# Kernel optimization log

Hardware: AMD Instinct MI355X
Metric: run time of the kernel (lower is better)

The kernel has to match this reference:

```python
import jax, jax.numpy as jnp
import numpy as np
import math

D_MODEL = 1024
N_HEADS = 16
D_HEAD = D_MODEL // N_HEADS
WINDOW = 256
SCALE = 1.0 / math.sqrt(D_HEAD)


def setup_inputs() -> dict:
    key = jax.random.key(0)
    kx, kqkv, kout = jax.random.split(key, 3)
    x = jax.random.normal(kx, (2, 2048, D_MODEL), dtype=jnp.float32)
    # xavier_uniform for nn.Linear weights (shape [out, in] in torch; store as [in, out] for x @ W)
    lim_qkv = math.sqrt(6.0 / (D_MODEL + 3 * D_MODEL))
    W_qkv = jax.random.uniform(kqkv, (D_MODEL, 3 * D_MODEL), dtype=jnp.float32, minval=-lim_qkv, maxval=lim_qkv)
    lim_out = math.sqrt(6.0 / (D_MODEL + D_MODEL))
    W_out = jax.random.uniform(kout, (D_MODEL, D_MODEL), dtype=jnp.float32, minval=-lim_out, maxval=lim_out)
    return {"x": x, "W_qkv": W_qkv, "W_out": W_out}


def _window_mask(seq_len: int) -> jnp.ndarray:
    # causal + sliding window: position i attends to j with i-WINDOW < j <= i
    i = jnp.arange(seq_len)[:, None]
    j = jnp.arange(seq_len)[None, :]
    allowed = (j <= i) & (j > i - WINDOW)
    return jnp.where(allowed, 0.0, -jnp.inf).astype(jnp.float32)


def reference(x, W_qkv, W_out):
    B, S, _ = x.shape
    qkv = x @ W_qkv                                   # [B, S, 3*D]
    qkv = qkv.reshape(B, S, 3, N_HEADS, D_HEAD)
    qkv = jnp.transpose(qkv, (2, 0, 3, 1, 4))         # [3, B, H, S, Dh]
    q, k, v = qkv[0], qkv[1], qkv[2]
    scores = jnp.einsum('bhsd,bhtd->bhst', q, k) * SCALE
    scores = scores + _window_mask(S)[None, None]
    weights = jax.nn.softmax(scores, axis=-1)
    out = jnp.einsum('bhst,bhtd->bhsd', weights, v)   # [B, H, S, Dh]
    out = jnp.transpose(out, (0, 2, 1, 3)).reshape(B, S, D_MODEL)
    return out @ W_out
```

## Files before the change

### kernel.cpp

```cpp
#include <hip/hip_runtime.h>

typedef unsigned short u16;
typedef unsigned int u32;

#define D_MODEL 1024
#define N_HEADS 16
#define D_HEAD 64
#define WIN 256
#define SEQ 2048
#define BATCH 2
#define NROWS (BATCH*SEQ)

typedef short frag_ab __attribute__((ext_vector_type(8)));
typedef float frag_cd __attribute__((ext_vector_type(4)));
typedef float f32x16 __attribute__((ext_vector_type(16)));
typedef u16 u16x8 __attribute__((ext_vector_type(8)));

__device__ __forceinline__ u16 f2bf(float f) {
    union { float f; u32 u; } x; x.f = f;
    u32 r = x.u + 0x7fffu + ((x.u >> 16) & 1u);
    return (u16)(r >> 16);
}

__device__ __forceinline__ void load_lds16(const void* g, void* l) {
    __builtin_amdgcn_global_load_lds(
        (const __attribute__((address_space(1))) void*)g,
        (__attribute__((address_space(3))) void*)l, 16, 0, 0);
}

__device__ __forceinline__ void transpose_tile(const float* __restrict__ W, u16* __restrict__ WT,
                                               int K, int N, int n0, int k0,
                                               int scale_rows, float scale, float (*tile)[33]) {
    int x = threadIdx.x & 31, y = threadIdx.x >> 5;
#pragma unroll
    for (int r = 0; r < 4; r++)
        tile[y + 8 * r][x] = W[(size_t)(k0 + y + 8 * r) * N + n0 + x];
    __syncthreads();
#pragma unroll
    for (int r = 0; r < 4; r++) {
        int nrow = n0 + y + 8 * r;
        float v = tile[x][y + 8 * r];
        if (nrow < scale_rows) v *= scale;
        WT[(size_t)nrow * K + k0 + x] = f2bf(v);
    }
}

__global__ __launch_bounds__(256) void prep_kernel(const float* __restrict__ x,
                                                   const float* __restrict__ W_qkv,
                                                   u16* __restrict__ xb,
                                                   u16* __restrict__ wqkvT,
                                                   float qscale) {
    __shared__ float tile[32][33];
    const int bid = blockIdx.x;
    if (bid < 4096) {
        int idx = bid * 256 + threadIdx.x;
        float4 v = ((const float4*)x)[idx];
        ushort4 o;
        o.x = f2bf(v.x); o.y = f2bf(v.y); o.z = f2bf(v.z); o.w = f2bf(v.w);
        ((ushort4*)xb)[idx] = o;
    } else {
        int t = bid - 4096;
        transpose_tile(W_qkv, wqkvT, D_MODEL, 3 * D_MODEL, (t % 96) * 32, (t / 96) * 32,
                       D_MODEL, qscale, tile);
    }
}

__global__ __launch_bounds__(512, 2) void gemm1_qkv(const u16* __restrict__ A,
                                                    const u16* __restrict__ BT,
                                                    u16* __restrict__ C) {
    constexpr int K = 1024, NLD = 3072, NT = K >> 6;
    __shared__ union SM {
        struct { u16 As[2][256 * 64]; u16 Bs[2][192 * 64]; } s;
        u16 cs[256 * 200];
    } sm;
    const int tid = threadIdx.x;
    const int xcd = blockIdx.x & 7, sblk = blockIdx.x >> 3;
    const int m0 = (sblk & 15) * 256;
    const int n0 = (xcd * 2 + (sblk >> 4)) * 192;
    const int wave = tid >> 6, lane = tid & 63;
    const int wm = (wave >> 1) * 64, wn = (wave & 1) * 96;
    const int l32 = lane & 31, kh = lane >> 5;

    const int r0 = tid >> 3;
    const int w  = (tid & 7) ^ (r0 & 7);
    const u16* aP = A  + (size_t)(m0 + r0) * K + w * 8;
    const u16* bP = BT + (size_t)(n0 + r0) * K + w * 8;

    f32x16 acc[2][3] = {};

#define STAGE(tile_, buf_) do {                                                   \
        const int k0_ = (tile_) * 64;                                             \
        _Pragma("unroll")                                                         \
        for (int u = 0; u < 4; ++u)                                               \
            load_lds16(aP + (size_t)(64 * u) * K + k0_,                           \
                       &sm.s.As[buf_][(tid + 512 * u) * 8]);                      \
        _Pragma("unroll")                                                         \
        for (int u = 0; u < 3; ++u)                                               \
            load_lds16(bP + (size_t)(64 * u) * K + k0_,                           \
                       &sm.s.Bs[buf_][(tid + 512 * u) * 8]);                      \
    } while (0)

    STAGE(0, 0);
    STAGE(1, 1);

    int cur = 0;
    for (int t = 0; t < NT; ++t) {
        if (t + 1 < NT) asm volatile("s_waitcnt vmcnt(7)" ::: "memory");
        else            asm volatile("s_waitcnt vmcnt(0)" ::: "memory");
        asm volatile("s_barrier" ::: "memory");

        const u16* As = sm.s.As[cur];
        const u16* Bs = sm.s.Bs[cur];
#pragma unroll
        for (int kk = 0; kk < 4; ++kk) {
            const int csel = ((kk * 2 + kh) ^ (l32 & 7)) * 8;
            frag_ab af[2], bf[3];
#pragma unroll
            for (int mt = 0; mt < 2; ++mt)
                af[mt] = *(const frag_ab*)&As[(wm + mt * 32 + l32) * 64 + csel];
#pragma unroll
            for (int nt = 0; nt < 3; ++nt)
                bf[nt] = *(const frag_ab*)&Bs[(wn + nt * 32 + l32) * 64 + csel];
            asm volatile("s_barrier" ::: "memory");
            __builtin_amdgcn_s_setprio(1);
#pragma unroll
            for (int mt = 0; mt < 2; ++mt)
#pragma unroll
                for (int nt = 0; nt < 3; ++nt)
                    acc[mt][nt] = __builtin_amdgcn_mfma_f32_32x32x16_bf16(
                        af[mt], bf[nt], acc[mt][nt], 0, 0, 0);
            __builtin_amdgcn_s_setprio(0);
            asm volatile("s_barrier" ::: "memory");
        }
        if (t + 2 < NT) STAGE(t + 2, cur);
        cur ^= 1;
    }
#undef STAGE

#pragma unroll
    for (int mt = 0; mt < 2; ++mt)
#pragma unroll
        for (int nt = 0; nt < 3; ++nt) {
            const int col = wn + nt * 32 + l32;
#pragma unroll
            for (int reg = 0; reg < 16; ++reg) {
                const int row = wm + mt * 32 + (reg & 3) + 8 * (reg >> 2) + 4 * kh;
                sm.cs[row * 200 + col] = f2bf(acc[mt][nt][reg]);
            }
        }
    asm volatile("s_barrier" ::: "memory");
#pragma unroll
    for (int i = 0; i < 12; ++i) {
        const int idx = tid + 512 * i;
        const int row = idx / 24, c8 = idx % 24;
        u16x8 vv = *(const u16x8*)&sm.cs[row * 200 + c8 * 8];
        *(u16x8*)(C + (size_t)(m0 + row) * NLD + n0 + c8 * 8) = vv;
    }
}

__global__ __launch_bounds__(256) void gemm2_out(const u16* __restrict__ A,
                                                 const u16* __restrict__ BT,
                                                 float* __restrict__ C) {
    constexpr int K = 1024, N = 1024, NT = K >> 6;
    __shared__ struct { u16 As[2][128 * 64]; u16 Bs[2][128 * 64]; } sm;
    const int tid = threadIdx.x;
    const int xcd = blockIdx.x & 7, sblk = blockIdx.x >> 3;
    const int m0 = sblk * 128;
    const int n0 = xcd * 128;
    const int wave = tid >> 6, lane = tid & 63;
    const int wm = (wave >> 1) * 64, wn = (wave & 1) * 64;
    const int l32 = lane & 31, kh = lane >> 5;

    const int r0 = tid >> 3;
    const int w  = (tid & 7) ^ (r0 & 7);
    const u16* aP = A  + (size_t)(m0 + r0) * K + w * 8;
    const u16* bP = BT + (size_t)(n0 + r0) * K + w * 8;

    f32x16 acc[2][2] = {};

#define STAGE2(tile_, buf_) do {                                                  \
        const int k0_ = (tile_) * 64;                                             \
        _Pragma("unroll")                                                         \
        for (int u = 0; u < 4; ++u)                                               \
            load_lds16(aP + (size_t)(32 * u) * K + k0_,                           \
                       &sm.As[buf_][(tid + 256 * u) * 8]);                        \
        _Pragma("unroll")                                                         \
        for (int u = 0; u < 4; ++u)                                               \
            load_lds16(bP + (size_t)(32 * u) * K + k0_,                           \
                       &sm.Bs[buf_][(tid + 256 * u) * 8]);                        \
    } while (0)

    STAGE2(0, 0);
    STAGE2(1, 1);

    int cur = 0;
    for (int t = 0; t < NT; ++t) {
        if (t + 1 < NT) asm volatile("s_waitcnt vmcnt(8)" ::: "memory");
        else            asm volatile("s_waitcnt vmcnt(0)" ::: "memory");
        asm volatile("s_barrier" ::: "memory");

        const u16* As = sm.As[cur];
        const u16* Bs = sm.Bs[cur];
#pragma unroll
        for (int ph = 0; ph < 2; ++ph) {
            frag_ab af[2][2], bf[2][2];
#pragma unroll
            for (int kx = 0; kx < 2; ++kx) {
                const int kk = ph * 2 + kx;
                const int csel = ((kk * 2 + kh) ^ (l32 & 7)) * 8;
#pragma unroll
                for (int mt = 0; mt < 2; ++mt)
                    af[kx][mt] = *(const frag_ab*)&As[(wm + mt * 32 + l32) * 64 + csel];
#pragma unroll
                for (int nt = 0; nt < 2; ++nt)
                    bf[kx][nt] = *(const frag_ab*)&Bs[(wn + nt * 32 + l32) * 64 + csel];
            }
            asm volatile("s_barrier" ::: "memory");
            __builtin_amdgcn_s_setprio(1);
#pragma unroll
            for (int kx = 0; kx < 2; ++kx)
#pragma unroll
                for (int mt = 0; mt < 2; ++mt)
#pragma unroll
                    for (int nt = 0; nt < 2; ++nt)
                        acc[mt][nt] = __builtin_amdgcn_mfma_f32_32x32x16_bf16(
                            af[kx][mt], bf[kx][nt], acc[mt][nt], 0, 0, 0);
            __builtin_amdgcn_s_setprio(0);
            asm volatile("s_barrier" ::: "memory");
        }
        if (t + 2 < NT) STAGE2(t + 2, cur);
        cur ^= 1;
    }
#undef STAGE2

#pragma unroll
    for (int mt = 0; mt < 2; ++mt)
#pragma unroll
        for (int nt = 0; nt < 2; ++nt) {
            const int col = n0 + wn + nt * 32 + l32;
#pragma unroll
            for (int reg = 0; reg < 16; ++reg) {
                const int row = m0 + wm + mt * 32 + (reg & 3) + 8 * (reg >> 2) + 4 * kh;
                C[(size_t)row * N + col] = acc[mt][nt][reg];
            }
        }
}

__global__ __launch_bounds__(256) void attn_kernel(const u16* __restrict__ qkv, u16* __restrict__ out,
                                                   const float* __restrict__ W_out,
                                                   u16* __restrict__ woutT) {
    __shared__ u16 Ks[2][64 * 64];
    __shared__ u16 Vt[64 * 72];
    __shared__ u16 ps[4][16 * 72];

    if (blockIdx.x >= 1024) {
        int t = blockIdx.x - 1024;
        transpose_tile(W_out, woutT, D_MODEL, D_MODEL, (t & 31) * 32, (t >> 5) * 32,
                       0, 1.0f, (float(*)[33])&Ks[0][0]);
        return;
    }

    const int tid = threadIdx.x;
    const int wave = tid >> 6, lane = tid & 63;
    const int quad = lane >> 4, c16 = lane & 15;

    const int bh = blockIdx.x & 31;
    const int qc = blockIdx.x >> 5;
    const int h  = bh & 15;
    const int b  = bh >> 4;
    const int q0 = qc * 64;
    const int qw0 = q0 + wave * 16;

    frag_ab qf[2];
    {
        const u16* qrow = qkv + (size_t)(b * SEQ + qw0 + c16) * 3072 + h * 64;
        qf[0] = *(const frag_ab*)(qrow + quad * 8);
        qf[1] = *(const frag_ab*)(qrow + 32 + quad * 8);
    }

    float m_r[4], l_r[4];
    frag_cd acc[4] = {};

    const int ntiles = qc < 4 ? qc + 1 : 5;

    const int krow = wave * 16 + (lane >> 3);
    const int kchunk = (lane & 7) ^ (lane >> 3);
    const int vj2 = (tid & 31) * 2, vd8 = tid >> 5;

    const u16* kbase = qkv + (size_t)(b * SEQ + krow) * 3072 + 1024 + h * 64 + kchunk * 8;
    const u16* vbase = qkv + (size_t)(b * SEQ + vj2) * 3072 + 2048 + h * 64 + vd8 * 8;

    u16x8 va, vb;
    {
        const u16* g = kbase + (size_t)q0 * 3072;
        load_lds16(g,            &Ks[0][krow * 64 + (lane & 7) * 8]);
        load_lds16(g + 8 * 3072, &Ks[0][(krow + 8) * 64 + (lane & 7) * 8]);
        const u16* gv = vbase + (size_t)q0 * 3072;
        va = *(const u16x8*)gv;
        vb = *(const u16x8*)(gv + 3072);
#pragma unroll
        for (int dd = 0; dd < 8; dd++)
            *(u32*)&Vt[(vd8 * 8 + dd) * 72 + vj2] = (u32)va[dd] | ((u32)vb[dd] << 16);
    }

    for (int t = 0; t < ntiles; t++) {
        const int cur = t & 1, nxt = cur ^ 1;
        const int j0 = q0 - 64 * t;
        __syncthreads();
        const bool pre = (t + 1 < ntiles);
        if (pre) {
            const u16* g = kbase + (size_t)(j0 - 64) * 3072;
            load_lds16(g,            &Ks[nxt][krow * 64 + (lane & 7) * 8]);
            load_lds16(g + 8 * 3072, &Ks[nxt][(krow + 8) * 64 + (lane & 7) * 8]);
            const u16* gv = vbase + (size_t)(j0 - 64) * 3072;
            va = *(const u16x8*)gv;
            vb = *(const u16x8*)(gv + 3072);
        }

        frag_cd s[4] = {};
#pragma unroll
        for (int kb = 0; kb < 4; kb++) {
            frag_ab kf0 = *(const frag_ab*)&Ks[cur][(kb * 16 + c16) * 64 + ((quad    ) ^ (c16 & 7)) * 8];
            frag_ab kf1 = *(const frag_ab*)&Ks[cur][(kb * 16 + c16) * 64 + ((4 + quad) ^ (c16 & 7)) * 8];
            s[kb] = __builtin_amdgcn_mfma_f32_16x16x32_bf16(qf[0], kf0, s[kb], 0, 0, 0);
            s[kb] = __builtin_amdgcn_mfma_f32_16x16x32_bf16(qf[1], kf1, s[kb], 0, 0, 0);
        }

        if (t == 0) {
#pragma unroll
            for (int reg = 0; reg < 4; reg++) {
                const int i = qw0 + quad * 4 + reg;
#pragma unroll
                for (int kb = 0; kb < 4; kb++)
                    if (q0 + kb * 16 + c16 > i) s[kb][reg] = -1e30f;
            }
        } else if (t == 4) {
#pragma unroll
            for (int reg = 0; reg < 4; reg++) {
                const int i = qw0 + quad * 4 + reg;
#pragma unroll
                for (int kb = 0; kb < 4; kb++)
                    if (j0 + kb * 16 + c16 + WIN <= i) s[kb][reg] = -1e30f;
            }
        }

        float mt_[4];
#pragma unroll
        for (int reg = 0; reg < 4; reg++)
            mt_[reg] = fmaxf(fmaxf(s[0][reg], s[1][reg]), fmaxf(s[2][reg], s[3][reg]));
#pragma unroll
        for (int off = 1; off < 16; off <<= 1)
#pragma unroll
            for (int reg = 0; reg < 4; reg++) mt_[reg] = fmaxf(mt_[reg], __shfl_xor(mt_[reg], off));

        float alpha[4];
        if (t == 0) {
#pragma unroll
            for (int reg = 0; reg < 4; reg++) m_r[reg] = mt_[reg];
        } else {
#pragma unroll
            for (int reg = 0; reg < 4; reg++) {
                float mn = fmaxf(m_r[reg], mt_[reg]);
                alpha[reg] = __builtin_amdgcn_exp2f(m_r[reg] - mn);
                m_r[reg] = mn;
            }
        }

        float rs[4] = {0.f, 0.f, 0.f, 0.f};
#pragma unroll
        for (int kb = 0; kb < 4; kb++)
#pragma unroll
            for (int reg = 0; reg < 4; reg++) {
                float p = __builtin_amdgcn_exp2f(s[kb][reg] - m_r[reg]);
                union { float f; u32 u; } pu; pu.f = p;
                ps[wave][(quad * 4 + reg) * 72 + kb * 16 + c16] = (u16)(pu.u >> 16);
                rs[reg] += p;
            }
#pragma unroll
        for (int off = 1; off < 16; off <<= 1)
#pragma unroll
            for (int reg = 0; reg < 4; reg++) rs[reg] += __shfl_xor(rs[reg], off);

        if (t == 0) {
#pragma unroll
            for (int reg = 0; reg < 4; reg++) l_r[reg] = rs[reg];
        } else {
#pragma unroll
            for (int reg = 0; reg < 4; reg++) l_r[reg] = l_r[reg] * alpha[reg] + rs[reg];
#pragma unroll
            for (int dblk = 0; dblk < 4; dblk++)
#pragma unroll
                for (int reg = 0; reg < 4; reg++) acc[dblk][reg] *= alpha[reg];
        }

#pragma unroll
        for (int js = 0; js < 2; js++) {
            frag_ab pf = *(const frag_ab*)&ps[wave][c16 * 72 + js * 32 + quad * 8];
#pragma unroll
            for (int dblk = 0; dblk < 4; dblk++) {
                frag_ab vf = *(const frag_ab*)&Vt[(dblk * 16 + c16) * 72 + js * 32 + quad * 8];
                acc[dblk] = __builtin_amdgcn_mfma_f32_16x16x32_bf16(pf, vf, acc[dblk], 0, 0, 0);
            }
        }

        if (pre) {
            __syncthreads();
#pragma unroll
            for (int dd = 0; dd < 8; dd++)
                *(u32*)&Vt[(vd8 * 8 + dd) * 72 + vj2] = (u32)va[dd] | ((u32)vb[dd] << 16);
        }
    }

    float inv[4];
#pragma unroll
    for (int reg = 0; reg < 4; reg++) inv[reg] = 1.f / l_r[reg];
#pragma unroll
    for (int dblk = 0; dblk < 4; dblk++)
#pragma unroll
        for (int reg = 0; reg < 4; reg++)
            out[(size_t)(b * SEQ + qw0 + quad * 4 + reg) * 1024 + h * 64 + dblk * 16 + c16] =
                f2bf(acc[dblk][reg] * inv[reg]);
}

extern "C" void kernel_launch(void* const* d_in, const int* in_sizes, int n_in,
                              void* d_out, int out_size, void* d_ws, size_t ws_size,
                              hipStream_t stream) {
    const float* x     = (const float*)d_in[0];
    const float* W_qkv = (const float*)d_in[1];
    const float* W_out = (const float*)d_in[2];
    float* out = (float*)d_out;

    char* ws = (char*)d_ws;
    u16* xb    = (u16*)(ws);
    u16* wqkvT = (u16*)(ws + 8388608);
    u16* woutT = (u16*)(ws + 14680064);
    u16* qkvb  = (u16*)(ws + 16777216);
    u16* attnb = (u16*)(ws + 41943040);

    const float QSCALE = 0.125f * 1.4426950408889634f;

    prep_kernel<<<7168, 256, 0, stream>>>(x, W_qkv, xb, wqkvT, QSCALE);
    gemm1_qkv<<<256, 512, 0, stream>>>(xb, wqkvT, qkvb);
    attn_kernel<<<2048, 256, 0, stream>>>(qkvb, attnb, W_out, woutT);
    gemm2_out<<<256, 256, 0, stream>>>(attnb, woutT, out);
}
```

Baseline: 149.8 us.

## Fuse QKV GEMM, attention and output GEMM into one persistent kernel with grid barriers

Merges gemm1, attention and gemm2 into a single persistent kernel of 256 blocks, separated by atomic-counter grid barriers, and moves the W_out transpose into the prep kernel. The goal is to remove launch gaps and tail effects between the three stages. In exchange, attention runs with only 256 blocks, two units each, instead of 2048 small blocks, and gemm2 moves to 512-thread blocks. The grid barriers also rely on all 256 blocks being co-resident on the GPU.

```diff
diff --git a/kernel.cpp b/kernel.cpp
--- a/kernel.cpp
+++ b/kernel.cpp
@@ -28,6 +28,19 @@
         (__attribute__((address_space(3))) void*)l, 16, 0, 0);
 }
 
+__device__ __forceinline__ void grid_sync(u32* cnt, u32 target) {
+    __syncthreads();
+    if (threadIdx.x == 0) {
+        __hip_atomic_fetch_add(cnt, 1u, __ATOMIC_RELEASE, __HIP_MEMORY_SCOPE_AGENT);
+        u32 v;
+        do {
+            __builtin_amdgcn_s_sleep(2);
+            v = __hip_atomic_load(cnt, __ATOMIC_ACQUIRE, __HIP_MEMORY_SCOPE_AGENT);
+        } while (v < target);
+    }
+    __syncthreads();
+}
+
 __device__ __forceinline__ void transpose_tile(const float* __restrict__ W, u16* __restrict__ WT,
                                                int K, int N, int n0, int k0,
                                                int scale_rows, float scale, float (*tile)[33]) {
@@ -47,227 +60,49 @@
 
 __global__ __launch_bounds__(256) void prep_kernel(const float* __restrict__ x,
                                                    const float* __restrict__ W_qkv,
+                                                   const float* __restrict__ W_out,
                                                    u16* __restrict__ xb,
                                                    u16* __restrict__ wqkvT,
+                                                   u16* __restrict__ woutT,
+                                                   u32* __restrict__ sync_cnt,
                                                    float qscale) {
     __shared__ float tile[32][33];
     const int bid = blockIdx.x;
+    if (bid == 0 && threadIdx.x == 0) *sync_cnt = 0;
     if (bid < 4096) {
         int idx = bid * 256 + threadIdx.x;
         float4 v = ((const float4*)x)[idx];
         ushort4 o;
         o.x = f2bf(v.x); o.y = f2bf(v.y); o.z = f2bf(v.z); o.w = f2bf(v.w);
         ((ushort4*)xb)[idx] = o;
-    } else {
+    } else if (bid < 7168) {
         int t = bid - 4096;
         transpose_tile(W_qkv, wqkvT, D_MODEL, 3 * D_MODEL, (t % 96) * 32, (t / 96) * 32,
                        D_MODEL, qscale, tile);
-    }
-}
-
-__global__ __launch_bounds__(512, 2) void gemm1_qkv(const u16* __restrict__ A,
-                                                    const u16* __restrict__ BT,
-                                                    u16* __restrict__ C) {
-    constexpr int K = 1024, NLD = 3072, NT = K >> 6;
-    __shared__ union SM {
-        struct { u16 As[2][256 * 64]; u16 Bs[2][192 * 64]; } s;
-        u16 cs[256 * 200];
-    } sm;
-    const int tid = threadIdx.x;
-    const int xcd = blockIdx.x & 7, sblk = blockIdx.x >> 3;
-    const int m0 = (sblk & 15) * 256;
-    const int n0 = (xcd * 2 + (sblk >> 4)) * 192;
-    const int wave = tid >> 6, lane = tid & 63;
-    const int wm = (wave >> 1) * 64, wn = (wave & 1) * 96;
-    const int l32 = lane & 31, kh = lane >> 5;
-
-    const int r0 = tid >> 3;
-    const int w  = (tid & 7) ^ (r0 & 7);
-    const u16* aP = A  + (size_t)(m0 + r0) * K + w * 8;
-    const u16* bP = BT + (size_t)(n0 + r0) * K + w * 8;
-
-    f32x16 acc[2][3] = {};
-
-#define STAGE(tile_, buf_) do {                                                   \
-        const int k0_ = (tile_) * 64;                                             \
-        _Pragma("unroll")                                                         \
-        for (int u = 0; u < 4; ++u)                                               \
-            load_lds16(aP + (size_t)(64 * u) * K + k0_,                           \
-                       &sm.s.As[buf_][(tid + 512 * u) * 8]);                      \
-        _Pragma("unroll")                                                         \
-        for (int u = 0; u < 3; ++u)                                               \
-            load_lds16(bP + (size_t)(64 * u) * K + k0_,                           \
-                       &sm.s.Bs[buf_][(tid + 512 * u) * 8]);                      \
-    } while (0)
-
-    STAGE(0, 0);
-    STAGE(1, 1);
-
-    int cur = 0;
-    for (int t = 0; t < NT; ++t) {
-        if (t + 1 < NT) asm volatile("s_waitcnt vmcnt(7)" ::: "memory");
-        else            asm volatile("s_waitcnt vmcnt(0)" ::: "memory");
-        asm volatile("s_barrier" ::: "memory");
-
-        const u16* As = sm.s.As[cur];
-        const u16* Bs = sm.s.Bs[cur];
-#pragma unroll
-        for (int kk = 0; kk < 4; ++kk) {
-            const int csel = ((kk * 2 + kh) ^ (l32 & 7)) * 8;
-            frag_ab af[2], bf[3];
-#pragma unroll
-            for (int mt = 0; mt < 2; ++mt)
-                af[mt] = *(const frag_ab*)&As[(wm + mt * 32 + l32) * 64 + csel];
-#pragma unroll
-            for (int nt = 0; nt < 3; ++nt)
-                bf[nt] = *(const frag_ab*)&Bs[(wn + nt * 32 + l32) * 64 + csel];
-            asm volatile("s_barrier" ::: "memory");
-            __builtin_amdgcn_s_setprio(1);
-#pragma unroll
-            for (int mt = 0; mt < 2; ++mt)
-#pragma unroll
-                for (int nt = 0; nt < 3; ++nt)
-                    acc[mt][nt] = __builtin_amdgcn_mfma_f32_32x32x16_bf16(
-                        af[mt], bf[nt], acc[mt][nt], 0, 0, 0);
-            __builtin_amdgcn_s_setprio(0);
-            asm volatile("s_barrier" ::: "memory");
-        }
-        if (t + 2 < NT) STAGE(t + 2, cur);
-        cur ^= 1;
-    }
-#undef STAGE
-
-#pragma unroll
-    for (int mt = 0; mt < 2; ++mt)
-#pragma unroll
-        for (int nt = 0; nt < 3; ++nt) {
-            const int col = wn + nt * 32 + l32;
-#pragma unroll
-            for (int reg = 0; reg < 16; ++reg) {
-                const int row = wm + mt * 32 + (reg & 3) + 8 * (reg >> 2) + 4 * kh;
-                sm.cs[row * 200 + col] = f2bf(acc[mt][nt][reg]);
-            }
-        }
-    asm volatile("s_barrier" ::: "memory");
-#pragma unroll
-    for (int i = 0; i < 12; ++i) {
-        const int idx = tid + 512 * i;
-        const int row = idx / 24, c8 = idx % 24;
-        u16x8 vv = *(const u16x8*)&sm.cs[row * 200 + c8 * 8];
-        *(u16x8*)(C + (size_t)(m0 + row) * NLD + n0 + c8 * 8) = vv;
-    }
-}
-
-__global__ __launch_bounds__(256) void gemm2_out(const u16* __restrict__ A,
-                                                 const u16* __restrict__ BT,
-                                                 float* __restrict__ C) {
-    constexpr int K = 1024, N = 1024, NT = K >> 6;
-    __shared__ struct { u16 As[2][128 * 64]; u16 Bs[2][128 * 64]; } sm;
-    const int tid = threadIdx.x;
-    const int xcd = blockIdx.x & 7, sblk = blockIdx.x >> 3;
-    const int m0 = sblk * 128;
-    const int n0 = xcd * 128;
-    const int wave = tid >> 6, lane = tid & 63;
-    const int wm = (wave >> 1) * 64, wn = (wave & 1) * 64;
-    const int l32 = lane & 31, kh = lane >> 5;
-
-    const int r0 = tid >> 3;
-    const int w  = (tid & 7) ^ (r0 & 7);
-    const u16* aP = A  + (size_t)(m0 + r0) * K + w * 8;
-    const u16* bP = BT + (size_t)(n0 + r0) * K + w * 8;
-
-    f32x16 acc[2][2] = {};
-
-#define STAGE2(tile_, buf_) do {                                                  \
-        const int k0_ = (tile_) * 64;                                             \
-        _Pragma("unroll")                                                         \
-        for (int u = 0; u < 4; ++u)                                               \
-            load_lds16(aP + (size_t)(32 * u) * K + k0_,                           \
-                       &sm.As[buf_][(tid + 256 * u) * 8]);                        \
-        _Pragma("unroll")                                                         \
-        for (int u = 0; u < 4; ++u)                                               \
-            load_lds16(bP + (size_t)(32 * u) * K + k0_,                           \
-                       &sm.Bs[buf_][(tid + 256 * u) * 8]);                        \
-    } while (0)
-
-    STAGE2(0, 0);
-    STAGE2(1, 1);
-
-    int cur = 0;
-    for (int t = 0; t < NT; ++t) {
-        if (t + 1 < NT) asm volatile("s_waitcnt vmcnt(8)" ::: "memory");
-        else            asm volatile("s_waitcnt vmcnt(0)" ::: "memory");
-        asm volatile("s_barrier" ::: "memory");
-
-        const u16* As = sm.As[cur];
-        const u16* Bs = sm.Bs[cur];
-#pragma unroll
-        for (int ph = 0; ph < 2; ++ph) {
-            frag_ab af[2][2], bf[2][2];
-#pragma unroll
-            for (int kx = 0; kx < 2; ++kx) {
-                const int kk = ph * 2 + kx;
-                const int csel = ((kk * 2 + kh) ^ (l32 & 7)) * 8;
-#pragma unroll
-                for (int mt = 0; mt < 2; ++mt)
-                    af[kx][mt] = *(const frag_ab*)&As[(wm + mt * 32 + l32) * 64 + csel];
-#pragma unroll
-                for (int nt = 0; nt < 2; ++nt)
-                    bf[kx][nt] = *(const frag_ab*)&Bs[(wn + nt * 32 + l32) * 64 + csel];
-            }
-            asm volatile("s_barrier" ::: "memory");
-            __builtin_amdgcn_s_setprio(1);
-#pragma unroll
-            for (int kx = 0; kx < 2; ++kx)
-#pragma unroll
-                for (int mt = 0; mt < 2; ++mt)
-#pragma unroll
-                    for (int nt = 0; nt < 2; ++nt)
-                        acc[mt][nt] = __builtin_amdgcn_mfma_f32_32x32x16_bf16(
-                            af[kx][mt], bf[kx][nt], acc[mt][nt], 0, 0, 0);
-            __builtin_amdgcn_s_setprio(0);
-            asm volatile("s_barrier" ::: "memory");
-        }
-        if (t + 2 < NT) STAGE2(t + 2, cur);
-        cur ^= 1;
-    }
-#undef STAGE2
-
-#pragma unroll
-    for (int mt = 0; mt < 2; ++mt)
-#pragma unroll
-        for (int nt = 0; nt < 2; ++nt) {
-            const int col = n0 + wn + nt * 32 + l32;
-#pragma unroll
-            for (int reg = 0; reg < 16; ++reg) {
-                const int row = m0 + wm + mt * 32 + (reg & 3) + 8 * (reg >> 2) + 4 * kh;
-                C[(size_t)row * N + col] = acc[mt][nt][reg];
-            }
-        }
-}
-
-__global__ __launch_bounds__(256) void attn_kernel(const u16* __restrict__ qkv, u16* __restrict__ out,
-                                                   const float* __restrict__ W_out,
-                                                   u16* __restrict__ woutT) {
-    __shared__ u16 Ks[2][64 * 64];
-    __shared__ u16 Vt[64 * 72];
-    __shared__ u16 ps[4][16 * 72];
-
-    if (blockIdx.x >= 1024) {
-        int t = blockIdx.x - 1024;
+    } else {
+        int t = bid - 7168;
         transpose_tile(W_out, woutT, D_MODEL, D_MODEL, (t & 31) * 32, (t >> 5) * 32,
-                       0, 1.0f, (float(*)[33])&Ks[0][0]);
-        return;
-    }
-
-    const int tid = threadIdx.x;
-    const int wave = tid >> 6, lane = tid & 63;
+                       0, 1.0f, tile);
+    }
+}
+
+struct AttnSM {
+    u16 Ks[2][64 * 64];
+    u16 Vt[64 * 72];
+    u16 ps[4][16 * 72];
+};
+
+union MegaSM {
+    struct { u16 As[2][256 * 64]; u16 Bs[2][192 * 64]; } g1;
+    u16 cs[256 * 200];
+    AttnSM at[2];
+    struct { u16 As[2][128 * 64]; u16 Bs[2][128 * 64]; } g2;
+};
+
+__device__ __forceinline__ void attn_unit(const u16* __restrict__ qkv, u16* __restrict__ out,
+                                          int b, int h, int qc, int t256, AttnSM* S) {
+    const int wave = t256 >> 6, lane = t256 & 63;
     const int quad = lane >> 4, c16 = lane & 15;
-
-    const int bh = blockIdx.x & 31;
-    const int qc = blockIdx.x >> 5;
-    const int h  = bh & 15;
-    const int b  = bh >> 4;
     const int q0 = qc * 64;
     const int qw0 = q0 + wave * 16;
 
@@ -285,7 +120,7 @@
 
     const int krow = wave * 16 + (lane >> 3);
     const int kchunk = (lane & 7) ^ (lane >> 3);
-    const int vj2 = (tid & 31) * 2, vd8 = tid >> 5;
+    const int vj2 = (t256 & 31) * 2, vd8 = t256 >> 5;
 
     const u16* kbase = qkv + (size_t)(b * SEQ + krow) * 3072 + 1024 + h * 64 + kchunk * 8;
     const u16* vbase = qkv + (size_t)(b * SEQ + vj2) * 3072 + 2048 + h * 64 + vd8 * 8;
@@ -293,14 +128,14 @@
     u16x8 va, vb;
     {
         const u16* g = kbase + (size_t)q0 * 3072;
-        load_lds16(g,            &Ks[0][krow * 64 + (lane & 7) * 8]);
-        load_lds16(g + 8 * 3072, &Ks[0][(krow + 8) * 64 + (lane & 7) * 8]);
+        load_lds16(g,            &S->Ks[0][krow * 64 + (lane & 7) * 8]);
+        load_lds16(g + 8 * 3072, &S->Ks[0][(krow + 8) * 64 + (lane & 7) * 8]);
         const u16* gv = vbase + (size_t)q0 * 3072;
         va = *(const u16x8*)gv;
         vb = *(const u16x8*)(gv + 3072);
 #pragma unroll
         for (int dd = 0; dd < 8; dd++)
-            *(u32*)&Vt[(vd8 * 8 + dd) * 72 + vj2] = (u32)va[dd] | ((u32)vb[dd] << 16);
+            *(u32*)&S->Vt[(vd8 * 8 + dd) * 72 + vj2] = (u32)va[dd] | ((u32)vb[dd] << 16);
     }
 
     for (int t = 0; t < ntiles; t++) {
@@ -310,8 +145,8 @@
         const bool pre = (t + 1 < ntiles);
         if (pre) {
             const u16* g = kbase + (size_t)(j0 - 64) * 3072;
-            load_lds16(g,            &Ks[nxt][krow * 64 + (lane & 7) * 8]);
-            load_lds16(g + 8 * 3072, &Ks[nxt][(krow + 8) * 64 + (lane & 7) * 8]);
+            load_lds16(g,            &S->Ks[nxt][krow * 64 + (lane & 7) * 8]);
+            load_lds16(g + 8 * 3072, &S->Ks[nxt][(krow + 8) * 64 + (lane & 7) * 8]);
             const u16* gv = vbase + (size_t)(j0 - 64) * 3072;
             va = *(const u16x8*)gv;
             vb = *(const u16x8*)(gv + 3072);
@@ -320,8 +155,8 @@
         frag_cd s[4] = {};
 #pragma unroll
         for (int kb = 0; kb < 4; kb++) {
-            frag_ab kf0 = *(const frag_ab*)&Ks[cur][(kb * 16 + c16) * 64 + ((quad    ) ^ (c16 & 7)) * 8];
-            frag_ab kf1 = *(const frag_ab*)&Ks[cur][(kb * 16 + c16) * 64 + ((4 + quad) ^ (c16 & 7)) * 8];
+            frag_ab kf0 = *(const frag_ab*)&S->Ks[cur][(kb * 16 + c16) * 64 + ((quad    ) ^ (c16 & 7)) * 8];
+            frag_ab kf1 = *(const frag_ab*)&S->Ks[cur][(kb * 16 + c16) * 64 + ((4 + quad) ^ (c16 & 7)) * 8];
             s[kb] = __builtin_amdgcn_mfma_f32_16x16x32_bf16(qf[0], kf0, s[kb], 0, 0, 0);
             s[kb] = __builtin_amdgcn_mfma_f32_16x16x32_bf16(qf[1], kf1, s[kb], 0, 0, 0);
         }
@@ -373,7 +208,7 @@
             for (int reg = 0; reg < 4; reg++) {
                 float p = __builtin_amdgcn_exp2f(s[kb][reg] - m_r[reg]);
                 union { float f; u32 u; } pu; pu.f = p;
-                ps[wave][(quad * 4 + reg) * 72 + kb * 16 + c16] = (u16)(pu.u >> 16);
+                S->ps[wave][(quad * 4 + reg) * 72 + kb * 16 + c16] = (u16)(pu.u >> 16);
                 rs[reg] += p;
             }
 #pragma unroll
@@ -395,10 +230,10 @@
 
 #pragma unroll
         for (int js = 0; js < 2; js++) {
-            frag_ab pf = *(const frag_ab*)&ps[wave][c16 * 72 + js * 32 + quad * 8];
+            frag_ab pf = *(const frag_ab*)&S->ps[wave][c16 * 72 + js * 32 + quad * 8];
 #pragma unroll
             for (int dblk = 0; dblk < 4; dblk++) {
-                frag_ab vf = *(const frag_ab*)&Vt[(dblk * 16 + c16) * 72 + js * 32 + quad * 8];
+                frag_ab vf = *(const frag_ab*)&S->Vt[(dblk * 16 + c16) * 72 + js * 32 + quad * 8];
                 acc[dblk] = __builtin_amdgcn_mfma_f32_16x16x32_bf16(pf, vf, acc[dblk], 0, 0, 0);
             }
         }
@@ -407,7 +242,7 @@
             __syncthreads();
 #pragma unroll
             for (int dd = 0; dd < 8; dd++)
-                *(u32*)&Vt[(vd8 * 8 + dd) * 72 + vj2] = (u32)va[dd] | ((u32)vb[dd] << 16);
+                *(u32*)&S->Vt[(vd8 * 8 + dd) * 72 + vj2] = (u32)va[dd] | ((u32)vb[dd] << 16);
         }
     }
 
@@ -420,6 +255,195 @@
         for (int reg = 0; reg < 4; reg++)
             out[(size_t)(b * SEQ + qw0 + quad * 4 + reg) * 1024 + h * 64 + dblk * 16 + c16] =
                 f2bf(acc[dblk][reg] * inv[reg]);
+}
+
+__global__ __launch_bounds__(512, 2) void mega_kernel(const u16* __restrict__ xb,
+                                                      const u16* __restrict__ wqkvT,
+                                                      u16* __restrict__ qkvb,
+                                                      u16* __restrict__ attnb,
+                                                      const u16* __restrict__ woutT,
+                                                      float* __restrict__ out,
+                                                      u32* __restrict__ sync_cnt) {
+    __shared__ MegaSM sm;
+    const int tid = threadIdx.x;
+    const int bid = blockIdx.x;
+    const int wave = tid >> 6, lane = tid & 63;
+    const int l32 = lane & 31, kh = lane >> 5;
+
+    {
+        constexpr int K = 1024, NLD = 3072, NT = K >> 6;
+        const int xcd = bid & 7, sblk = bid >> 3;
+        const int m0 = (sblk & 15) * 256;
+        const int n0 = (xcd * 2 + (sblk >> 4)) * 192;
+        const int wm = (wave >> 1) * 64, wn = (wave & 1) * 96;
+
+        const int r0 = tid >> 3;
+        const int w  = (tid & 7) ^ (r0 & 7);
+        const u16* aP = xb    + (size_t)(m0 + r0) * K + w * 8;
+        const u16* bP = wqkvT + (size_t)(n0 + r0) * K + w * 8;
+
+        f32x16 acc[2][3] = {};
+
+#define STAGE1(tile_, buf_) do {                                                  \
+        const int k0_ = (tile_) * 64;                                             \
+        _Pragma("unroll")                                                         \
+        for (int u = 0; u < 4; ++u)                                               \
+            load_lds16(aP + (size_t)(64 * u) * K + k0_,                           \
+                       &sm.g1.As[buf_][(tid + 512 * u) * 8]);                     \
+        _Pragma("unroll")                                                         \
+        for (int u = 0; u < 3; ++u)                                               \
+            load_lds16(bP + (size_t)(64 * u) * K + k0_,                           \
+                       &sm.g1.Bs[buf_][(tid + 512 * u) * 8]);                     \
+    } while (0)
+
+        STAGE1(0, 0);
+        STAGE1(1, 1);
+
+        int cur = 0;
+        for (int t = 0; t < NT; ++t) {
+            if (t + 1 < NT) asm volatile("s_waitcnt vmcnt(7)" ::: "memory");
+            else            asm volatile("s_waitcnt vmcnt(0)" ::: "memory");
+            asm volatile("s_barrier" ::: "memory");
+
+            const u16* As = sm.g1.As[cur];
+            const u16* Bs = sm.g1.Bs[cur];
+#pragma unroll
+            for (int kk = 0; kk < 4; ++kk) {
+                const int csel = ((kk * 2 + kh) ^ (l32 & 7)) * 8;
+                frag_ab af[2], bf[3];
+#pragma unroll
+                for (int mt = 0; mt < 2; ++mt)
+                    af[mt] = *(const frag_ab*)&As[(wm + mt * 32 + l32) * 64 + csel];
+#pragma unroll
+                for (int nt = 0; nt < 3; ++nt)
+                    bf[nt] = *(const frag_ab*)&Bs[(wn + nt * 32 + l32) * 64 + csel];
+                asm volatile("s_barrier" ::: "memory");
+                __builtin_amdgcn_s_setprio(1);
+#pragma unroll
+                for (int mt = 0; mt < 2; ++mt)
+#pragma unroll
+                    for (int nt = 0; nt < 3; ++nt)
+                        acc[mt][nt] = __builtin_amdgcn_mfma_f32_32x32x16_bf16(
+                            af[mt], bf[nt], acc[mt][nt], 0, 0, 0);
+                __builtin_amdgcn_s_setprio(0);
+                asm volatile("s_barrier" ::: "memory");
+            }
+            if (t + 2 < NT) STAGE1(t + 2, cur);
+            cur ^= 1;
+        }
+#undef STAGE1
+
+#pragma unroll
+        for (int mt = 0; mt < 2; ++mt)
+#pragma unroll
+            for (int nt = 0; nt < 3; ++nt) {
+                const int col = wn + nt * 32 + l32;
+#pragma unroll
+                for (int reg = 0; reg < 16; ++reg) {
+                    const int row = wm + mt * 32 + (reg & 3) + 8 * (reg >> 2) + 4 * kh;
+                    sm.cs[row * 200 + col] = f2bf(acc[mt][nt][reg]);
+                }
+            }
+        asm volatile("s_barrier" ::: "memory");
+#pragma unroll
+        for (int i = 0; i < 12; ++i) {
+            const int idx = tid + 512 * i;
+            const int row = idx / 24, c8 = idx % 24;
+            u16x8 vv = *(const u16x8*)&sm.cs[row * 200 + c8 * 8];
+            *(u16x8*)(qkvb + (size_t)(m0 + row) * NLD + n0 + c8 * 8) = vv;
+        }
+    }
+
+    grid_sync(sync_cnt, 256);
+
+    {
+        const int hh = tid >> 8, t256 = tid & 255;
+        const int bh = (bid & 7) + 8 * ((bid >> 3) & 1) + 16 * hh;
+        const int h = bh & 15, b = bh >> 4;
+        const int qcbase = (bid >> 4) * 2;
+#pragma unroll 1
+        for (int r = 0; r < 2; ++r) {
+            __syncthreads();
+            attn_unit(qkvb, attnb, b, h, qcbase + r, t256, &sm.at[hh]);
+        }
+    }
+
+    grid_sync(sync_cnt, 512);
+
+    {
+        constexpr int K = 1024, N = 1024, NT = K >> 6;
+        const int xcd = bid & 7, sblk = bid >> 3;
+        const int m0 = sblk * 128, n0 = xcd * 128;
+        const int wm = (wave >> 2) * 64, wn = (wave & 3) * 32;
+
+        const int r0 = tid >> 3;
+        const int w  = (tid & 7) ^ (r0 & 7);
+        const u16* aP = attnb + (size_t)(m0 + r0) * K + w * 8;
+        const u16* bP = woutT + (size_t)(n0 + r0) * K + w * 8;
+
+        f32x16 acc[2] = {};
+
+#define STAGE3(tile_, buf_) do {                                                  \
+        const int k0_ = (tile_) * 64;                                             \
+        _Pragma("unroll")                                                         \
+        for (int u = 0; u < 2; ++u)                                               \
+            load_lds16(aP + (size_t)(64 * u) * K + k0_,                           \
+                       &sm.g2.As[buf_][(tid + 512 * u) * 8]);                     \
+        _Pragma("unroll")                                                         \
+        for (int u = 0; u < 2; ++u)                                               \
+            load_lds16(bP + (size_t)(64 * u) * K + k0_,                           \
+                       &sm.g2.Bs[buf_][(tid + 512 * u) * 8]);                     \
+    } while (0)
+
+        STAGE3(0, 0);
+        STAGE3(1, 1);
+
+        int cur = 0;
+        for (int t = 0; t < NT; ++t) {
+            if (t + 1 < NT) asm volatile("s_waitcnt vmcnt(4)" ::: "memory");
+            else            asm volatile("s_waitcnt vmcnt(0)" ::: "memory");
+            asm volatile("s_barrier" ::: "memory");
+
+            const u16* As = sm.g2.As[cur];
+            const u16* Bs = sm.g2.Bs[cur];
+#pragma unroll
+            for (int ph = 0; ph < 2; ++ph) {
+                frag_ab af[2][2], bf[2];
+#pragma unroll
+                for (int kx = 0; kx < 2; ++kx) {
+                    const int kk = ph * 2 + kx;
+                    const int csel = ((kk * 2 + kh) ^ (l32 & 7)) * 8;
+#pragma unroll
+                    for (int mt = 0; mt < 2; ++mt)
+                        af[kx][mt] = *(const frag_ab*)&As[(wm + mt * 32 + l32) * 64 + csel];
+                    bf[kx] = *(const frag_ab*)&Bs[(wn + l32) * 64 + csel];
+                }
+                asm volatile("s_barrier" ::: "memory");
+                __builtin_amdgcn_s_setprio(1);
+#pragma unroll
+                for (int kx = 0; kx < 2; ++kx)
+#pragma unroll
+                    for (int mt = 0; mt < 2; ++mt)
+                        acc[mt] = __builtin_amdgcn_mfma_f32_32x32x16_bf16(
+                            af[kx][mt], bf[kx], acc[mt], 0, 0, 0);
+                __builtin_amdgcn_s_setprio(0);
+                asm volatile("s_barrier" ::: "memory");
+            }
+            if (t + 2 < NT) STAGE3(t + 2, cur);
+            cur ^= 1;
+        }
+#undef STAGE3
+
+#pragma unroll
+        for (int mt = 0; mt < 2; ++mt) {
+            const int col = n0 + wn + l32;
+#pragma unroll
+            for (int reg = 0; reg < 16; ++reg) {
+                const int row = m0 + wm + mt * 32 + (reg & 3) + 8 * (reg >> 2) + 4 * kh;
+                out[(size_t)row * N + col] = acc[mt][reg];
+            }
+        }
+    }
 }
 
 extern "C" void kernel_launch(void* const* d_in, const int* in_sizes, int n_in,
@@ -436,11 +460,10 @@
     u16* woutT = (u16*)(ws + 14680064);
     u16* qkvb  = (u16*)(ws + 16777216);
     u16* attnb = (u16*)(ws + 41943040);
+    u32* scnt  = (u32*)(ws + 67108864);
 
     const float QSCALE = 0.125f * 1.4426950408889634f;
 
-    prep_kernel<<<7168, 256, 0, stream>>>(x, W_qkv, xb, wqkvT, QSCALE);
-    gemm1_qkv<<<256, 512, 0, stream>>>(xb, wqkvT, qkvb);
-    attn_kernel<<<2048, 256, 0, stream>>>(qkvb, attnb, W_out, woutT);
-    gemm2_out<<<256, 256, 0, stream>>>(attnb, woutT, out);
-}
+    prep_kernel<<<8192, 256, 0, stream>>>(x, W_qkv, W_out, xb, wqkvT, woutT, scnt, QSCALE);
+    mega_kernel<<<256, 512, 0, stream>>>(xb, wqkvT, qkvb, attnb, woutT, out, scnt);
+}
```

Measured after the change: 204.9 us. 1.37x slower.
